# Performance work log

Hardware: AMD Instinct MI355X
Metric: run time of the kernel (lower is better)

The kernel has to match this reference:

```python
import math
import jax, jax.numpy as jnp
import numpy as np

B, T, D, M, S = 2, 4096, 1024, 256, 8
BEAM = 4
TAU = 1.0


def setup_inputs() -> dict:
    key = jax.random.key(0)
    ks = jax.random.split(key, 24)
    std = 0.02
    inp = {
        "mu": jax.random.normal(ks[0], (B, T, D), jnp.float32),
        "lam": jax.random.uniform(ks[1], (B, T, D), jnp.float32),
        "pi": jax.random.uniform(ks[2], (B, T, 7), jnp.float32),
        "pi_write": jax.random.uniform(ks[3], (B, T, 1), jnp.float32),
        "Wq": jax.random.normal(ks[4], (M, D), jnp.float32) * std,
        "bq": jnp.zeros((M,), jnp.float32),
        "Wk": jax.random.normal(ks[5], (M, D), jnp.float32) * std,
        "bk": jnp.zeros((M,), jnp.float32),
        "Wv": jax.random.normal(ks[6], (M, D), jnp.float32) * std,
        "bv": jnp.zeros((M,), jnp.float32),
        "Wo": jax.random.normal(ks[7], (D, M), jnp.float32) * std,
        "bo": jnp.zeros((D,), jnp.float32),
        "Ws1": jax.random.normal(ks[8], (256, 2 * D + 7), jnp.float32) * std,
        "bs1": jnp.zeros((256,), jnp.float32),
        "Ws2": jax.random.normal(ks[9], (1, 256), jnp.float32) * std,
        "bs2": jnp.zeros((1,), jnp.float32),
        "Wsr": jax.random.normal(ks[10], (M, M), jnp.float32) * std,
        "bsr": jnp.zeros((M,), jnp.float32),
        "scratch_init": jax.random.normal(ks[11], (1, S, M), jnp.float32) * 0.02,
        "gate": jnp.float32(-5.0),
    }
    return inp


def _build_tree(k, v, w):
    """Causal binary tree of weighted span summaries. Level 0 = leaves."""
    levels = [(k, v, w)]
    while k.shape[1] > 1:
        n = k.shape[1]
        if n % 2 == 1:
            pad = ((0, 0), (0, 1), (0, 0))
            k = jnp.pad(k, pad); v = jnp.pad(v, pad); w = jnp.pad(w, pad)
        k1, k2 = k[:, 0::2], k[:, 1::2]
        v1, v2 = v[:, 0::2], v[:, 1::2]
        w1, w2 = w[:, 0::2], w[:, 1::2]
        tw = w1 + w2 + 1e-8
        k = (w1 * k1 + w2 * k2) / tw
        v = (w1 * v1 + w2 * v2) / tw
        w = tw
        levels.append((k, v, w))
    return levels


def _retrieve_at_level(q, keys, values, beam):
    Bq, Tq, Mq = q.shape
    n = keys.shape[1]
    scores = jnp.einsum('btm,bnm->btn', q, keys) / math.sqrt(Mq)
    if n <= Tq:  # causal: query i may only see slot j <= i
        mask = jnp.arange(n)[None, :] > jnp.arange(Tq)[:, None]
        scores = jnp.where(mask[None], -jnp.inf, scores)
    kk = min(beam, n)
    if n > kk:
        vals, idx = jax.lax.top_k(scores, kk)           # (B,T,k)
        p = jax.nn.softmax(vals, axis=-1)               # == softmax of scattered sparse scores
        v_sel = jnp.take_along_axis(values[:, None], idx[..., None], axis=2)  # (B,T,k,M)
        return jnp.einsum('btk,btkm->btm', p, v_sel)
    attn = jax.nn.softmax(scores, axis=-1)
    return jnp.einsum('btn,bnm->btm', attn, values)


def reference(mu, lam, pi, pi_write, Wq, bq, Wk, bk, Wv, bv, Wo, bo,
              Ws1, bs1, Ws2, bs2, Wsr, bsr, scratch_init, gate):
    # ---- write: build causal tree from detached keys/values ----
    mu_d = jax.lax.stop_gradient(mu)
    w0 = jax.lax.stop_gradient(pi_write)                # (B,T,1)
    k = mu_d @ Wk.T + bk
    v = mu_d @ Wv.T + bv
    tree = _build_tree(k, v, w0)

    # ---- read ----
    q = mu @ Wq.T + bq                                  # (B,T,M)
    log_var = -jnp.log(jnp.clip(lam, 1e-6))
    si = jnp.concatenate([mu, log_var, pi], axis=-1)    # (B,T,2D+7)
    h = si @ Ws1.T + bs1
    h = h * jax.nn.sigmoid(h)                           # SiLU
    s = jax.nn.sigmoid((h @ Ws2.T + bs2)[..., 0])       # (B,T)

    scratch = jnp.broadcast_to(scratch_init, (mu.shape[0], S, M))
    sq = q @ Wsr.T + bsr
    sattn = jax.nn.softmax(jnp.einsum('btm,bsm->bts', sq, scratch) / math.sqrt(M), axis=-1)
    scratch_ctx = jnp.einsum('bts,bsm->btm', sattn, scratch)

    level_ctx = [_retrieve_at_level(q, lk, lv, BEAM) for (lk, lv, _) in tree]
    level_stack = jnp.stack(level_ctx, axis=2)          # (B,T,L,M)
    L = level_stack.shape[2]
    level_idx = jnp.arange(L, dtype=mu.dtype)
    s_scaled = s[..., None] * (L - 1)                   # (B,T,1)
    kappa = jnp.exp(-0.5 * ((level_idx - s_scaled) / TAU) ** 2)
    kappa = kappa / jnp.clip(kappa.sum(axis=-1, keepdims=True), 1e-8)
    tree_ctx = jnp.einsum('btl,btlm->btm', kappa, level_stack)

    blend = s[..., None]
    combined = (1.0 - blend) * tree_ctx + blend * scratch_ctx
    out = combined @ Wo.T + bo
    return jax.nn.sigmoid(gate) * out                   # (B,T,D)
```

## Files before the change

### kernel.cpp

```cpp
#include <hip/hip_runtime.h>
#include <math.h>

#define TT 4096
#define BB 2
#define MMDIM 256
#define RTOT 8192
#define NSLICE 39

typedef __attribute__((ext_vector_type(8))) short short8_t;
typedef __attribute__((ext_vector_type(4))) float f32x4;

__global__ __launch_bounds__(256) void gemm_f32(
    const float* __restrict__ A, const float* __restrict__ W,
    const float* __restrict__ bias, float* __restrict__ C, int K, int N)
{
    __shared__ float As[16][68];
    __shared__ float Ws[16][68];
    const int tid = threadIdx.x;
    const int tx = tid & 15, ty = tid >> 4;
    const int r0 = blockIdx.x * 64, c0 = blockIdx.y * 64;
    const int lr = tid >> 2;
    const int lk = (tid & 3) << 2;

    float acc[4][4] = {};

    for (int k0 = 0; k0 < K; k0 += 16) {
        float4 av = *(const float4*)&A[(size_t)(r0 + lr) * K + k0 + lk];
        float4 wv = *(const float4*)&W[(size_t)(c0 + lr) * K + k0 + lk];
        As[lk + 0][lr] = av.x; As[lk + 1][lr] = av.y;
        As[lk + 2][lr] = av.z; As[lk + 3][lr] = av.w;
        Ws[lk + 0][lr] = wv.x; Ws[lk + 1][lr] = wv.y;
        Ws[lk + 2][lr] = wv.z; Ws[lk + 3][lr] = wv.w;
        __syncthreads();
        #pragma unroll
        for (int kk = 0; kk < 16; ++kk) {
            float4 a = *(const float4*)&As[kk][ty * 4];
            float4 b = *(const float4*)&Ws[kk][tx * 4];
            acc[0][0] += a.x * b.x; acc[0][1] += a.x * b.y; acc[0][2] += a.x * b.z; acc[0][3] += a.x * b.w;
            acc[1][0] += a.y * b.x; acc[1][1] += a.y * b.y; acc[1][2] += a.y * b.z; acc[1][3] += a.y * b.w;
            acc[2][0] += a.z * b.x; acc[2][1] += a.z * b.y; acc[2][2] += a.z * b.z; acc[2][3] += a.z * b.w;
            acc[3][0] += a.w * b.x; acc[3][1] += a.w * b.y; acc[3][2] += a.w * b.z; acc[3][3] += a.w * b.w;
        }
        __syncthreads();
    }

    #pragma unroll
    for (int i = 0; i < 4; ++i) {
        int row = r0 + ty * 4 + i;
        float4 o;
        o.x = acc[i][0] + bias[c0 + tx * 4 + 0];
        o.y = acc[i][1] + bias[c0 + tx * 4 + 1];
        o.z = acc[i][2] + bias[c0 + tx * 4 + 2];
        o.w = acc[i][3] + bias[c0 + tx * 4 + 3];
        *(float4*)&C[(size_t)row * N + c0 + tx * 4] = o;
    }
}

__device__ __forceinline__ unsigned short f2bf(float x)
{
    unsigned u = __float_as_uint(x);
    u += 0x7fffu + ((u >> 16) & 1u);
    return (unsigned short)(u >> 16);
}

__global__ __launch_bounds__(256) void convert_split(
    const float* __restrict__ src, unsigned short* __restrict__ hi,
    unsigned short* __restrict__ lo, int n4)
{
    int i = blockIdx.x * 256 + threadIdx.x;
    if (i >= n4) return;
    float4 x = ((const float4*)src)[i];
    ushort4 h, l;
    h.x = f2bf(x.x); l.x = f2bf(x.x - __uint_as_float((unsigned)h.x << 16));
    h.y = f2bf(x.y); l.y = f2bf(x.y - __uint_as_float((unsigned)h.y << 16));
    h.z = f2bf(x.z); l.z = f2bf(x.z - __uint_as_float((unsigned)h.z << 16));
    h.w = f2bf(x.w); l.w = f2bf(x.w - __uint_as_float((unsigned)h.w << 16));
    ((ushort4*)hi)[i] = h;
    ((ushort4*)lo)[i] = l;
}

__global__ __launch_bounds__(256) void pad_ws1_split(
    const float* __restrict__ src, unsigned short* __restrict__ hi,
    unsigned short* __restrict__ lo)
{
    const int r = blockIdx.x;
    for (int c = threadIdx.x; c < 2112; c += 256) {
        float v = (c < 2055) ? src[(size_t)r * 2055 + c] : 0.f;
        unsigned short h = f2bf(v);
        hi[(size_t)r * 2112 + c] = h;
        lo[(size_t)r * 2112 + c] = f2bf(v - __uint_as_float((unsigned)h << 16));
    }
}

template<int ASRC, int WITH_GATE>
__global__ __launch_bounds__(256) void gemm_mfma(
    const float* __restrict__ A, const float* __restrict__ lam,
    const float* __restrict__ pi,
    const unsigned short* __restrict__ Wh, const unsigned short* __restrict__ Wl,
    const float* __restrict__ bias, const float* __restrict__ gate,
    float* __restrict__ C, int K, int N)
{
    __shared__ unsigned short Ah[64][72], Al[64][72];
    __shared__ unsigned short Bh[128][72], Bl[128][72];
    const int tid = threadIdx.x;
    const int lane = tid & 63;
    const int wv = tid >> 6;
    const int r0 = blockIdx.x * 64;
    const int c0 = blockIdx.y * 128;

    f32x4 acc0[8] = {}, acc1[8] = {}, acc2[8] = {};

    const int arow = wv * 16 + (lane & 15);
    const int koff = (lane >> 4) * 8;

    for (int kc = 0; kc < K; kc += 64) {
        #pragma unroll
        for (int i = 0; i < 2; ++i) {
            int g = tid + i * 256;
            int row = g >> 3, gq = g & 7;
            float x[8];
            if (ASRC == 0) {
                float4 v0 = *(const float4*)&A[(size_t)(r0 + row) * K + kc + gq * 8];
                float4 v1 = *(const float4*)&A[(size_t)(r0 + row) * K + kc + gq * 8 + 4];
                x[0] = v0.x; x[1] = v0.y; x[2] = v0.z; x[3] = v0.w;
                x[4] = v1.x; x[5] = v1.y; x[6] = v1.z; x[7] = v1.w;
            } else {
                #pragma unroll
                for (int e = 0; e < 8; ++e) {
                    int c = kc + gq * 8 + e;
                    float val;
                    if (c < 1024)      val = A[(size_t)(r0 + row) * 1024 + c];
                    else if (c < 2048) val = -logf(fmaxf(lam[(size_t)(r0 + row) * 1024 + (c - 1024)], 1e-6f));
                    else if (c < 2055) val = pi[(size_t)(r0 + row) * 7 + (c - 2048)];
                    else               val = 0.f;
                    x[e] = val;
                }
            }
            short8_t sh, sl;
            #pragma unroll
            for (int e = 0; e < 8; ++e) {
                unsigned short h = f2bf(x[e]);
                sh[e] = (short)h;
                sl[e] = (short)f2bf(x[e] - __uint_as_float((unsigned)h << 16));
            }
            *(short8_t*)&Ah[row][gq * 8] = sh;
            *(short8_t*)&Al[row][gq * 8] = sl;
        }
        #pragma unroll
        for (int i = 0; i < 4; ++i) {
            int g = tid + i * 256;
            int row = g >> 3, gq = g & 7;
            *(short8_t*)&Bh[row][gq * 8] = *(const short8_t*)&Wh[(size_t)(c0 + row) * K + kc + gq * 8];
            *(short8_t*)&Bl[row][gq * 8] = *(const short8_t*)&Wl[(size_t)(c0 + row) * K + kc + gq * 8];
        }
        __syncthreads();
        #pragma unroll
        for (int kt = 0; kt < 2; ++kt) {
            short8_t afh = *(const short8_t*)&Ah[arow][kt * 32 + koff];
            short8_t afl = *(const short8_t*)&Al[arow][kt * 32 + koff];
            #pragma unroll
            for (int ct = 0; ct < 8; ++ct) {
                short8_t bh = *(const short8_t*)&Bh[ct * 16 + (lane & 15)][kt * 32 + koff];
                short8_t bl = *(const short8_t*)&Bl[ct * 16 + (lane & 15)][kt * 32 + koff];
                acc0[ct] = __builtin_amdgcn_mfma_f32_16x16x32_bf16(afh, bh, acc0[ct], 0, 0, 0);
                acc1[ct] = __builtin_amdgcn_mfma_f32_16x16x32_bf16(afl, bh, acc1[ct], 0, 0, 0);
                acc2[ct] = __builtin_amdgcn_mfma_f32_16x16x32_bf16(afh, bl, acc2[ct], 0, 0, 0);
            }
        }
        __syncthreads();
    }

    float g = 1.f;
    if (WITH_GATE) g = 1.f / (1.f + expf(-gate[0]));
    #pragma unroll
    for (int ct = 0; ct < 8; ++ct) {
        int col = c0 + ct * 16 + (lane & 15);
        float b = bias[col];
        #pragma unroll
        for (int r = 0; r < 4; ++r) {
            int row = r0 + wv * 16 + (lane >> 4) * 4 + r;
            C[(size_t)row * N + col] = (acc0[ct][r] + acc1[ct][r] + acc2[ct][r] + b) * g;
        }
    }
}

__global__ __launch_bounds__(256) void s_kernel(
    const float* __restrict__ h, const float* __restrict__ Ws2,
    const float* __restrict__ bs2, float* __restrict__ sb,
    float* __restrict__ kap)
{
    const int tid = threadIdx.x;
    const int wave = tid >> 6, lane = tid & 63;
    const int t = blockIdx.x * 4 + wave;

    float4 hv = *(const float4*)&h[(size_t)t * MMDIM + lane * 4];
    float4 wv = *(const float4*)&Ws2[lane * 4];
    float p = 0.f;
    p += (hv.x / (1.f + expf(-hv.x))) * wv.x;
    p += (hv.y / (1.f + expf(-hv.y))) * wv.y;
    p += (hv.z / (1.f + expf(-hv.z))) * wv.z;
    p += (hv.w / (1.f + expf(-hv.w))) * wv.w;
    #pragma unroll
    for (int o = 32; o; o >>= 1) p += __shfl_xor(p, o);

    float z = p + bs2[0];
    float s = 1.f / (1.f + expf(-z));
    float c = s * 12.f;
    float Z = 0.f;
    #pragma unroll
    for (int l = 0; l < 13; ++l) {
        float d = (float)l - c;
        Z += expf(-0.5f * d * d);
    }
    Z = fmaxf(Z, 1e-8f);
    if (lane < 13) {
        float d = (float)lane - c;
        kap[(size_t)t * 16 + lane] = (1.f - s) * expf(-0.5f * d * d) / Z;
    }
    if (lane == 0) sb[t] = s;
}

__global__ __launch_bounds__(256) void scratch_kernel(
    const float* __restrict__ sq, const float* __restrict__ scr,
    const float* __restrict__ sb, float* __restrict__ ctx)
{
    const int tid = threadIdx.x;
    const int wave = tid >> 6, lane = tid & 63;
    const int t = blockIdx.x * 4 + wave;

    float4 qv = *(const float4*)&sq[(size_t)t * MMDIM + lane * 4];
    float4 fr[8];
    float sc[8];
    #pragma unroll
    for (int s = 0; s < 8; ++s) {
        fr[s] = *(const float4*)&scr[s * MMDIM + lane * 4];
        sc[s] = qv.x * fr[s].x + qv.y * fr[s].y + qv.z * fr[s].z + qv.w * fr[s].w;
    }
    #pragma unroll
    for (int s = 0; s < 8; ++s) {
        #pragma unroll
        for (int o = 32; o; o >>= 1) sc[s] += __shfl_xor(sc[s], o);
        sc[s] *= 0.0625f;
    }
    float mx = sc[0];
    #pragma unroll
    for (int s = 1; s < 8; ++s) mx = fmaxf(mx, sc[s]);
    float sum = 0.f;
    #pragma unroll
    for (int s = 0; s < 8; ++s) { sc[s] = expf(sc[s] - mx); sum += sc[s]; }
    float inv = 1.f / sum;
    float blend = sb[t];
    float4 o = {0, 0, 0, 0};
    #pragma unroll
    for (int s = 0; s < 8; ++s) {
        float pp = sc[s] * inv;
        o.x += pp * fr[s].x; o.y += pp * fr[s].y;
        o.z += pp * fr[s].z; o.w += pp * fr[s].w;
    }
    o.x *= blend; o.y *= blend; o.z *= blend; o.w *= blend;
    *(float4*)&ctx[(size_t)t * MMDIM + lane * 4] = o;
}

__global__ __launch_bounds__(256) void wtree_kernel(
    const float* __restrict__ pw, float* __restrict__ wtree)
{
    __shared__ float wa[4096];
    __shared__ float wb2[2048];
    const int b = blockIdx.x;
    const int tid = threadIdx.x;
    for (int t = tid; t < 4096; t += 256) wa[t] = pw[b * 4096 + t];
    __syncthreads();
    int n = 4096, lvl = 1;
    float* cur = wa; float* nxt = wb2;
    while (n > 1) {
        int nout = n >> 1;
        int off = TT - (8192 >> lvl);
        for (int j = tid; j < nout; j += 256) {
            float t = cur[2 * j] + cur[2 * j + 1] + 1e-8f;
            nxt[j] = t;
            wtree[b * 4095 + off + j] = t;
        }
        __syncthreads();
        float* tmp = cur; cur = nxt; nxt = tmp;
        n = nout; ++lvl;
    }
}

__global__ __launch_bounds__(256) void tree_level(
    const float* __restrict__ kin, const float* __restrict__ vin,
    const float* __restrict__ win, float* __restrict__ kout,
    float* __restrict__ vout, int in_bs, int win_bs, int out_bs)
{
    const int j = blockIdx.x;
    const int b = blockIdx.y;
    const int tid = threadIdx.x;
    const float* wp = win + (size_t)b * win_bs;
    float w1 = wp[2 * j], w2 = wp[2 * j + 1];
    float tw = w1 + w2 + 1e-8f;
    size_t i1 = ((size_t)b * in_bs + 2 * j) * MMDIM + tid;
    size_t io = ((size_t)b * out_bs + j) * MMDIM + tid;
    kout[io] = (w1 * kin[i1] + w2 * kin[i1 + MMDIM]) / tw;
    vout[io] = (w1 * vin[i1] + w2 * vin[i1 + MMDIM]) / tw;
}

__global__ __launch_bounds__(256) void tree_mid(
    float* __restrict__ kt_, float* __restrict__ vt_,
    const float* __restrict__ wtree)
{
    __shared__ float kb[128][68];
    __shared__ float vb[128][68];
    const int tid = threadIdx.x;
    const int g  = blockIdx.x >> 2;
    const int mc = blockIdx.x & 3;
    const int b  = blockIdx.y;
    const int wb = b * 4095;

    for (int idx = tid; idx < 64 * 64; idx += 256) {
        int j = idx >> 6, m = idx & 63;
        size_t gi = (size_t)(wb + g * 64 + j) * MMDIM + mc * 64 + m;
        kb[j][m] = kt_[gi];
        vb[j][m] = vt_[gi];
    }
    __syncthreads();

    int pb = 0;
    for (int l = 2; l <= 6; ++l) {
        int nloc = 64 >> (l - 1);
        int cb = 128 - (128 >> (l - 1));
        int offm1 = TT - (8192 >> (l - 1));
        int offl  = TT - (8192 >> l);
        int gbase = g * nloc;
        for (int idx = tid; idx < nloc * 64; idx += 256) {
            int j = idx >> 6, m = idx & 63;
            float w1 = wtree[wb + offm1 + (gbase + j) * 2];
            float w2 = wtree[wb + offm1 + (gbase + j) * 2 + 1];
            float tw = wtree[wb + offl + gbase + j];
            float kvv = (w1 * kb[pb + 2 * j][m] + w2 * kb[pb + 2 * j + 1][m]) / tw;
            float vvv = (w1 * vb[pb + 2 * j][m] + w2 * vb[pb + 2 * j + 1][m]) / tw;
            kb[cb + j][m] = kvv;
            vb[cb + j][m] = vvv;
            size_t go = (size_t)(wb + offl + gbase + j) * MMDIM + mc * 64 + m;
            kt_[go] = kvv;
            vt_[go] = vvv;
        }
        __syncthreads();
        pb = cb;
    }
}

__global__ __launch_bounds__(256) void tree_deep(
    float* __restrict__ kt_, float* __restrict__ vt_,
    const float* __restrict__ wtree)
{
    __shared__ float kb[128][68];
    __shared__ float vb[128][68];
    const int tid = threadIdx.x;
    const int mc = blockIdx.x;
    const int b = blockIdx.y;
    const int wb = b * 4095;

    for (int idx = tid; idx < 64 * 64; idx += 256) {
        int j = idx >> 6, m = idx & 63;
        size_t gi = (size_t)(wb + 3968 + j) * MMDIM + mc * 64 + m;
        kb[j][m] = kt_[gi];
        vb[j][m] = vt_[gi];
    }
    __syncthreads();

    int pb = 0;
    for (int l = 7; l <= 12; ++l) {
        int nout = 4096 >> l;
        int cb = 128 - (128 >> (l - 6));
        int offm1 = TT - (8192 >> (l - 1));
        int offl  = TT - (8192 >> l);
        for (int idx = tid; idx < nout * 64; idx += 256) {
            int j = idx >> 6, m = idx & 63;
            float w1 = wtree[wb + offm1 + 2 * j];
            float w2 = wtree[wb + offm1 + 2 * j + 1];
            float tw = wtree[wb + offl + j];
            float kvv = (w1 * kb[pb + 2 * j][m] + w2 * kb[pb + 2 * j + 1][m]) / tw;
            float vvv = (w1 * vb[pb + 2 * j][m] + w2 * vb[pb + 2 * j + 1][m]) / tw;
            kb[cb + j][m] = kvv;
            vb[cb + j][m] = vvv;
            size_t go = (size_t)(wb + offl + j) * MMDIM + mc * 64 + m;
            kt_[go] = kvv;
            vt_[go] = vvv;
        }
        __syncthreads();
        pb = cb;
    }
}

__device__ __forceinline__ unsigned long long pack_key(float v, int col)
{
    unsigned u = __float_as_uint(v);
    u ^= ((unsigned)((int)u >> 31)) | 0x80000000u;
    return ((unsigned long long)u << 32) | (unsigned)(~col);
}

__device__ __forceinline__ void unpack_key(unsigned long long k, float& v, int& col)
{
    unsigned u = (unsigned)(k >> 32);
    u ^= (u & 0x80000000u) ? 0x80000000u : 0xFFFFFFFFu;
    v = __uint_as_float(u);
    col = (int)(~(unsigned)k);
}

__device__ __forceinline__ unsigned long long shfl_xor_u64(unsigned long long v, int off)
{
    int lo = __shfl_xor((int)(unsigned)v, off);
    int hi = __shfl_xor((int)(v >> 32), off);
    return ((unsigned long long)(unsigned)hi << 32) | (unsigned)lo;
}

__device__ __forceinline__ void ins4u(unsigned long long k, unsigned long long t[4])
{
    if (k <= t[3]) return;
    t[3] = k;
    if (t[3] > t[2]) { unsigned long long x = t[2]; t[2] = t[3]; t[3] = x; }
    if (t[2] > t[1]) { unsigned long long x = t[1]; t[1] = t[2]; t[2] = x; }
    if (t[1] > t[0]) { unsigned long long x = t[0]; t[0] = t[1]; t[1] = x; }
}

__device__ __forceinline__ void ins5u(unsigned long long k, unsigned long long t[5])
{
    if (k <= t[4]) return;
    t[4] = k;
    if (t[4] > t[3]) { unsigned long long x = t[3]; t[3] = t[4]; t[4] = x; }
    if (t[3] > t[2]) { unsigned long long x = t[2]; t[2] = t[3]; t[3] = x; }
    if (t[2] > t[1]) { unsigned long long x = t[1]; t[1] = t[2]; t[2] = x; }
    if (t[1] > t[0]) { unsigned long long x = t[0]; t[0] = t[1]; t[1] = x; }
}

__device__ __forceinline__ bool beats(float v, int id, float v2, int id2)
{
    return (v > v2) || (v == v2 && id < id2);
}

__device__ __forceinline__ void ins5(float v, int id, float tv[5], int ti[5])
{
    if (!beats(v, id, tv[4], ti[4])) return;
    tv[4] = v; ti[4] = id;
    #pragma unroll
    for (int s = 4; s > 0; --s) {
        if (beats(tv[s], ti[s], tv[s - 1], ti[s - 1])) {
            float fv = tv[s]; tv[s] = tv[s - 1]; tv[s - 1] = fv;
            int iv = ti[s]; ti[s] = ti[s - 1]; ti[s - 1] = iv;
        }
    }
}

__device__ __forceinline__ void slice_map(int sid, int& level, int& c0)
{
    if (sid < 16)      { level = 0; c0 = sid << 8; }
    else if (sid < 24) { level = 1; c0 = (sid - 16) << 8; }
    else if (sid < 28) { level = 2; c0 = (sid - 24) << 8; }
    else if (sid < 30) { level = 3; c0 = (sid - 28) << 8; }
    else               { level = sid - 26; c0 = 0; }
}

__global__ __launch_bounds__(512) void topk_mfma(
    const unsigned short* __restrict__ qkh, const unsigned short* __restrict__ qkl,
    const unsigned short* __restrict__ kth, const unsigned short* __restrict__ ktl,
    float2* __restrict__ topw)
{
    __shared__ unsigned short kbh[32][264];
    __shared__ unsigned short kbl[32][264];

    const int tid = threadIdx.x;
    const int lane = tid & 63;
    const int wv = tid >> 6;
    const int r0 = blockIdx.x * 128;
    const int sid = blockIdx.y;
    const int b = r0 >> 12;
    const int t0 = r0 & 4095;

    int level, c0b;
    slice_map(sid, level, c0b);
    const int n = TT >> level;
    const int nv = min(min(n, t0 + 128), c0b + 256);

    if (c0b >= nv) {
        if (tid < 128) {
            float2 e = make_float2(-INFINITY, __int_as_float(0x7fffffff));
            #pragma unroll
            for (int s = 0; s < 5; ++s)
                topw[(size_t)(sid * 5 + s) * RTOT + r0 + tid] = e;
        }
        return;
    }

    const unsigned short* Kh;
    const unsigned short* Kl;
    if (level == 0) {
        Kh = qkh + (size_t)RTOT * MMDIM + (size_t)b * TT * MMDIM;
        Kl = qkl + (size_t)RTOT * MMDIM + (size_t)b * TT * MMDIM;
    } else {
        size_t off = (size_t)b * 4095 + (TT - (8192 >> level));
        Kh = kth + off * MMDIM;
        Kl = ktl + off * MMDIM;
    }

    const int arow = r0 + wv * 16 + (lane & 15);
    const int koff = (lane >> 4) * 8;
    short8_t ah[8], al[8];
    #pragma unroll
    for (int kt = 0; kt < 8; ++kt) {
        ah[kt] = *(const short8_t*)(qkh + (size_t)arow * MMDIM + kt * 32 + koff);
        al[kt] = *(const short8_t*)(qkl + (size_t)arow * MMDIM + kt * 32 + koff);
    }

    unsigned long long tk[4][4] = {};
    const int trow0 = t0 + wv * 16 + (lane >> 4) * 4;

    const int scol = tid >> 4;
    const int kseg = (tid & 15) * 16;

    for (int c0 = c0b; c0 < nv; c0 += 32) {
        {
            int cc = min(c0 + scol, n - 1);
            const unsigned short* gh = Kh + (size_t)cc * MMDIM + kseg;
            const unsigned short* gl = Kl + (size_t)cc * MMDIM + kseg;
            *(short8_t*)&kbh[scol][kseg]     = *(const short8_t*)gh;
            *(short8_t*)&kbh[scol][kseg + 8] = *(const short8_t*)(gh + 8);
            *(short8_t*)&kbl[scol][kseg]     = *(const short8_t*)gl;
            *(short8_t*)&kbl[scol][kseg + 8] = *(const short8_t*)(gl + 8);
        }
        __syncthreads();

        #pragma unroll
        for (int ct = 0; ct < 2; ++ct) {
            f32x4 a0 = {0.f, 0.f, 0.f, 0.f};
            f32x4 a1 = {0.f, 0.f, 0.f, 0.f};
            f32x4 a2 = {0.f, 0.f, 0.f, 0.f};
            const int bc = ct * 16 + (lane & 15);
            #pragma unroll
            for (int kt = 0; kt < 8; ++kt) {
                short8_t bh = *(const short8_t*)&kbh[bc][kt * 32 + koff];
                short8_t bl = *(const short8_t*)&kbl[bc][kt * 32 + koff];
                a0 = __builtin_amdgcn_mfma_f32_16x16x32_bf16(ah[kt], bh, a0, 0, 0, 0);
                a1 = __builtin_amdgcn_mfma_f32_16x16x32_bf16(al[kt], bh, a1, 0, 0, 0);
                a2 = __builtin_amdgcn_mfma_f32_16x16x32_bf16(ah[kt], bl, a2, 0, 0, 0);
            }
            const int col = c0 + bc;
            #pragma unroll
            for (int r = 0; r < 4; ++r) {
                float sc = (a0[r] + a1[r] + a2[r]) * 0.0625f;
                unsigned long long key =
                    (col <= trow0 + r && col < n) ? pack_key(sc, col) : 0ull;
                if (__any(key > tk[r][3])) ins4u(key, tk[r]);
            }
        }
        __syncthreads();
    }

    #pragma unroll
    for (int r = 0; r < 4; ++r) {
        unsigned long long k5[5];
        #pragma unroll
        for (int s = 0; s < 4; ++s) k5[s] = tk[r][s];
        k5[4] = 0ull;
        #pragma unroll
        for (int pass = 0; pass < 4; ++pass) {
            int off = 1 << pass;
            unsigned long long o[5];
            #pragma unroll
            for (int s = 0; s < 5; ++s) o[s] = shfl_xor_u64(k5[s], off);
            #pragma unroll
            for (int s = 0; s < 5; ++s) ins5u(o[s], k5);
        }
        if ((lane & 15) == 0) {
            int row = r0 + wv * 16 + (lane >> 4) * 4 + r;
            #pragma unroll
            for (int s = 0; s < 5; ++s) {
                float2 e;
                if (k5[s] == 0ull) {
                    e = make_float2(-INFINITY, __int_as_float(0x7fffffff));
                } else {
                    float v; int c;
                    unpack_key(k5[s], v, c);
                    e = make_float2(v, __int_as_float(c));
                }
                topw[(size_t)(sid * 5 + s) * RTOT + row] = e;
            }
        }
    }
}

__global__ __launch_bounds__(256) void merge_gather(
    const float2* __restrict__ topw, const float* __restrict__ q,
    const float* __restrict__ kl0, const float* __restrict__ ktf,
    const float* __restrict__ vl0, const float* __restrict__ vtree,
    const float* __restrict__ kap, float* __restrict__ ctx)
{
    const int tid = threadIdx.x;
    const int lane = tid & 63;
    const int wv = __builtin_amdgcn_readfirstlane(tid >> 6);
    const int row = blockIdx.x * 4 + wv;
    const int b = row >> 12;

    float cr[4] = {0, 0, 0, 0};
    const float4 q4 = *(const float4*)&q[(size_t)row * MMDIM + lane * 4];

    for (int l = 0; l <= 12; ++l) {
        int s0, cnt;
        if (l == 0)      { s0 = 0;  cnt = 16; }
        else if (l == 1) { s0 = 16; cnt = 8; }
        else if (l == 2) { s0 = 24; cnt = 4; }
        else if (l == 3) { s0 = 28; cnt = 2; }
        else             { s0 = 26 + l; cnt = 1; }

        float tv[5]; int ti[5];
        #pragma unroll
        for (int s = 0; s < 5; ++s) { tv[s] = -INFINITY; ti[s] = 0x7fffffff; }
        for (int sl = 0; sl < cnt; ++sl) {
            #pragma unroll
            for (int s = 0; s < 5; ++s) {
                float2 e = topw[(size_t)((s0 + sl) * 5 + s) * RTOT + row];
                if (e.x > -INFINITY) ins5(e.x, __float_as_int(e.y), tv, ti);
            }
        }

        const float* Kf = (l == 0)
            ? kl0 + (size_t)b * TT * MMDIM
            : ktf + ((size_t)b * 4095 + (TT - (8192 >> l))) * MMDIM;

        bool ambig = (l <= 9) && (tv[3] - tv[4] < 1e-4f);
        if (ambig) {
            float rv[5]; int ri[5];
            #pragma unroll
            for (int s = 0; s < 5; ++s) { rv[s] = -INFINITY; ri[s] = 0x7fffffff; }
            for (int sl = 0; sl < cnt; ++sl) {
                #pragma unroll
                for (int s = 0; s < 5; ++s) {
                    float2 e = topw[(size_t)((s0 + sl) * 5 + s) * RTOT + row];
                    if (e.x > -INFINITY) {
                        int idx = __float_as_int(e.y);
                        float4 k4 = *(const float4*)&Kf[(size_t)idx * MMDIM + lane * 4];
                        float p = q4.x * k4.x + q4.y * k4.y + q4.z * k4.z + q4.w * k4.w;
                        #pragma unroll
                        for (int o = 32; o; o >>= 1) p += __shfl_xor(p, o);
                        ins5(p * 0.0625f, idx, rv, ri);
                    }
                }
            }
            #pragma unroll
            for (int s = 0; s < 5; ++s) { tv[s] = rv[s]; ti[s] = ri[s]; }
        }

        float m0 = tv[0];
        float e0 = expf(tv[0] - m0);
        float e1 = expf(tv[1] - m0);
        float e2 = expf(tv[2] - m0);
        float e3 = expf(tv[3] - m0);
        float sum = e0 + e1 + e2 + e3;
        float kp = kap[(size_t)row * 16 + l];
        float scl = kp / sum;
        float ps[4] = {e0 * scl, e1 * scl, e2 * scl, e3 * scl};

        const float* Vb = (l == 0)
            ? vl0 + (size_t)b * TT * MMDIM
            : vtree + ((size_t)b * 4095 + (TT - (8192 >> l))) * MMDIM;

        #pragma unroll
        for (int s = 0; s < 4; ++s) {
            if (ps[s] > 0.f) {
                float4 vv = *(const float4*)&Vb[(size_t)ti[s] * MMDIM + lane * 4];
                cr[0] += ps[s] * vv.x; cr[1] += ps[s] * vv.y;
                cr[2] += ps[s] * vv.z; cr[3] += ps[s] * vv.w;
            }
        }
    }

    float* cp = ctx + (size_t)row * MMDIM + lane * 4;
    float4 c = *(float4*)cp;
    c.x += cr[0]; c.y += cr[1]; c.z += cr[2]; c.w += cr[3];
    *(float4*)cp = c;
}

extern "C" void kernel_launch(void* const* d_in, const int* in_sizes, int n_in,
                              void* d_out, int out_size, void* d_ws, size_t ws_size,
                              hipStream_t stream)
{
    const float* mu  = (const float*)d_in[0];
    const float* lam = (const float*)d_in[1];
    const float* pi  = (const float*)d_in[2];
    const float* pw  = (const float*)d_in[3];
    const float* Wq  = (const float*)d_in[4];
    const float* bq  = (const float*)d_in[5];
    const float* Wk  = (const float*)d_in[6];
    const float* bk  = (const float*)d_in[7];
    const float* Wv  = (const float*)d_in[8];
    const float* bv  = (const float*)d_in[9];
    const float* Wo  = (const float*)d_in[10];
    const float* bo  = (const float*)d_in[11];
    const float* Ws1 = (const float*)d_in[12];
    const float* bs1 = (const float*)d_in[13];
    const float* Ws2 = (const float*)d_in[14];
    const float* bs2 = (const float*)d_in[15];
    const float* Wsr = (const float*)d_in[16];
    const float* bsr = (const float*)d_in[17];
    const float* scr = (const float*)d_in[18];
    const float* gate = (const float*)d_in[19];
    float* out = (float*)d_out;

    float* w = (float*)d_ws;
    const size_t RM = (size_t)RTOT * MMDIM;
    float* q_   = w;  w += RM;
    float* k_   = w;  w += RM;
    float* v_   = w;  w += RM;
    float* h_   = w;  w += RM;
    float* sq_  = w;  w += RM;
    float* ctx_ = w;  w += RM;
    float* sb_  = w;  w += RTOT;
    float* kap_ = w;  w += (size_t)RTOT * 16;
    float* kt_  = w;  w += (size_t)BB * 4095 * MMDIM;
    float* vt_  = w;  w += (size_t)BB * 4095 * MMDIM;
    float* wtree_ = w; w += (size_t)BB * 4095;
    unsigned short* qkh_ = (unsigned short*)w;  w += RM;
    unsigned short* qkl_ = (unsigned short*)w;  w += RM;
    unsigned short* kth_ = (unsigned short*)w;  w += (size_t)BB * 4095 * MMDIM / 2;
    unsigned short* ktl_ = (unsigned short*)w;  w += (size_t)BB * 4095 * MMDIM / 2;
    float2* topw = (float2*)w;  w += (size_t)NSLICE * 5 * RTOT * 2;
    unsigned short* w1h_ = (unsigned short*)w;  w += (size_t)256 * 2112 / 2;
    unsigned short* w1l_ = (unsigned short*)w;  w += (size_t)256 * 2112 / 2;
    unsigned short* wvh_ = (unsigned short*)w;  w += (size_t)256 * 1024 / 2;
    unsigned short* wvl_ = (unsigned short*)w;  w += (size_t)256 * 1024 / 2;
    unsigned short* wsrh_ = (unsigned short*)w; w += (size_t)256 * 256 / 2;
    unsigned short* wsrl_ = (unsigned short*)w; w += (size_t)256 * 256 / 2;
    unsigned short* woh_ = (unsigned short*)w;  w += (size_t)1024 * 256 / 2;
    unsigned short* wol_ = (unsigned short*)w;  w += (size_t)1024 * 256 / 2;

    pad_ws1_split<<<256, 256, 0, stream>>>(Ws1, w1h_, w1l_);
    convert_split<<<256, 256, 0, stream>>>(Wv, wvh_, wvl_, 65536);
    convert_split<<<64, 256, 0, stream>>>(Wsr, wsrh_, wsrl_, 16384);
    convert_split<<<256, 256, 0, stream>>>(Wo, woh_, wol_, 65536);

    gemm_f32<<<dim3(128, 4), 256, 0, stream>>>(mu, Wq, bq, q_, 1024, 256);
    gemm_f32<<<dim3(128, 4), 256, 0, stream>>>(mu, Wk, bk, k_, 1024, 256);
    gemm_mfma<0, 0><<<dim3(128, 2), 256, 0, stream>>>(mu, nullptr, nullptr, wvh_, wvl_,
                                                      bv, nullptr, v_, 1024, 256);
    gemm_mfma<1, 0><<<dim3(128, 2), 256, 0, stream>>>(mu, lam, pi, w1h_, w1l_,
                                                      bs1, nullptr, h_, 2112, 256);
    s_kernel<<<2048, 256, 0, stream>>>(h_, Ws2, bs2, sb_, kap_);
    gemm_mfma<0, 0><<<dim3(128, 2), 256, 0, stream>>>(q_, nullptr, nullptr, wsrh_, wsrl_,
                                                      bsr, nullptr, sq_, 256, 256);
    scratch_kernel<<<2048, 256, 0, stream>>>(sq_, scr, sb_, ctx_);

    wtree_kernel<<<BB, 256, 0, stream>>>(pw, wtree_);
    tree_level<<<dim3(2048, BB), 256, 0, stream>>>(k_, v_, pw, kt_, vt_,
                                                   TT, TT, 4095);
    tree_mid<<<dim3(128, BB), 256, 0, stream>>>(kt_, vt_, wtree_);
    tree_deep<<<dim3(4, BB), 256, 0, stream>>>(kt_, vt_, wtree_);

    convert_split<<<(int)((2 * RM / 4 + 255) / 256), 256, 0, stream>>>(
        q_, qkh_, qkl_, (int)(2 * RM / 4));
    convert_split<<<(int)(((size_t)BB * 4095 * MMDIM / 4 + 255) / 256), 256, 0, stream>>>(
        kt_, kth_, ktl_, (int)((size_t)BB * 4095 * MMDIM / 4));

    topk_mfma<<<dim3(64, NSLICE), 512, 0, stream>>>(qkh_, qkl_, kth_, ktl_, topw);
    merge_gather<<<2048, 256, 0, stream>>>(topw, q_, k_, kt_, v_, vt_, kap_, ctx_);
    gemm_mfma<0, 1><<<dim3(128, 8), 256, 0, stream>>>(ctx_, nullptr, nullptr, woh_, wol_,
                                                      bo, gate, out, 256, 1024);
}
```

Measured before the change: 899.9 us.

## Fuse Q/K projections with bf16 split conversion and double-buffer top-k tiles

Replaces the two separate fp32 GEMM launches for Q and K with one kernel that uses 64x128 tiles, register-prefetched double-buffered shared memory, and writes the hi/lo bf16 split of q and k directly. This removes one convert_split pass over q/k and one kernel launch. The top-k MFMA kernel also gains double-buffered LDS for key tiles, prefetching the next tile into registers while computing the current one, so it needs only one barrier per iteration. The cost is doubled LDS use in topk_mfma, which may reduce occupancy.

```diff
diff --git a/kernel.cpp b/kernel.cpp
--- a/kernel.cpp
+++ b/kernel.cpp
@@ -10,57 +10,104 @@
 typedef __attribute__((ext_vector_type(8))) short short8_t;
 typedef __attribute__((ext_vector_type(4))) float f32x4;
 
-__global__ __launch_bounds__(256) void gemm_f32(
-    const float* __restrict__ A, const float* __restrict__ W,
-    const float* __restrict__ bias, float* __restrict__ C, int K, int N)
-{
-    __shared__ float As[16][68];
-    __shared__ float Ws[16][68];
-    const int tid = threadIdx.x;
-    const int tx = tid & 15, ty = tid >> 4;
-    const int r0 = blockIdx.x * 64, c0 = blockIdx.y * 64;
-    const int lr = tid >> 2;
-    const int lk = (tid & 3) << 2;
-
-    float acc[4][4] = {};
-
-    for (int k0 = 0; k0 < K; k0 += 16) {
-        float4 av = *(const float4*)&A[(size_t)(r0 + lr) * K + k0 + lk];
-        float4 wv = *(const float4*)&W[(size_t)(c0 + lr) * K + k0 + lk];
-        As[lk + 0][lr] = av.x; As[lk + 1][lr] = av.y;
-        As[lk + 2][lr] = av.z; As[lk + 3][lr] = av.w;
-        Ws[lk + 0][lr] = wv.x; Ws[lk + 1][lr] = wv.y;
-        Ws[lk + 2][lr] = wv.z; Ws[lk + 3][lr] = wv.w;
-        __syncthreads();
-        #pragma unroll
-        for (int kk = 0; kk < 16; ++kk) {
-            float4 a = *(const float4*)&As[kk][ty * 4];
-            float4 b = *(const float4*)&Ws[kk][tx * 4];
-            acc[0][0] += a.x * b.x; acc[0][1] += a.x * b.y; acc[0][2] += a.x * b.z; acc[0][3] += a.x * b.w;
-            acc[1][0] += a.y * b.x; acc[1][1] += a.y * b.y; acc[1][2] += a.y * b.z; acc[1][3] += a.y * b.w;
-            acc[2][0] += a.z * b.x; acc[2][1] += a.z * b.y; acc[2][2] += a.z * b.z; acc[2][3] += a.z * b.w;
-            acc[3][0] += a.w * b.x; acc[3][1] += a.w * b.y; acc[3][2] += a.w * b.z; acc[3][3] += a.w * b.w;
-        }
-        __syncthreads();
-    }
-
-    #pragma unroll
-    for (int i = 0; i < 4; ++i) {
-        int row = r0 + ty * 4 + i;
-        float4 o;
-        o.x = acc[i][0] + bias[c0 + tx * 4 + 0];
-        o.y = acc[i][1] + bias[c0 + tx * 4 + 1];
-        o.z = acc[i][2] + bias[c0 + tx * 4 + 2];
-        o.w = acc[i][3] + bias[c0 + tx * 4 + 3];
-        *(float4*)&C[(size_t)row * N + c0 + tx * 4] = o;
-    }
-}
-
 __device__ __forceinline__ unsigned short f2bf(float x)
 {
     unsigned u = __float_as_uint(x);
     u += 0x7fffu + ((u >> 16) & 1u);
     return (unsigned short)(u >> 16);
+}
+
+__global__ __launch_bounds__(256) void gemm_qk(
+    const float* __restrict__ mu, const float* __restrict__ Wq,
+    const float* __restrict__ bq, const float* __restrict__ Wk,
+    const float* __restrict__ bk, float* __restrict__ q_, float* __restrict__ k_,
+    unsigned short* __restrict__ qkh, unsigned short* __restrict__ qkl)
+{
+    __shared__ float As[2][8][68];
+    __shared__ float Ws[2][8][132];
+    const int tid = threadIdx.x;
+    const int tx = tid & 15;
+    const int ty = tid >> 4;
+    const int r0 = blockIdx.x * 64;
+    const int c0 = blockIdx.y * 128;
+    const bool isq = (c0 < 256);
+
+    const float* W = isq ? (Wq + (size_t)c0 * 1024)
+                         : (Wk + (size_t)(c0 - 256) * 1024);
+    const float* bias = isq ? (bq + c0) : (bk + (c0 - 256));
+
+    const bool isA = (tid < 128);
+    const int sArow = tid >> 1, sAk = (tid & 1) * 4;
+    const int sWrow = tid >> 1, sWk = (tid & 1) * 4;
+
+    float acc[4][8] = {};
+    float4 rA, rW;
+
+    if (isA) rA = *(const float4*)&mu[(size_t)(r0 + sArow) * 1024 + sAk];
+    rW = *(const float4*)&W[(size_t)sWrow * 1024 + sWk];
+    if (isA) {
+        As[0][sAk + 0][sArow] = rA.x; As[0][sAk + 1][sArow] = rA.y;
+        As[0][sAk + 2][sArow] = rA.z; As[0][sAk + 3][sArow] = rA.w;
+    }
+    Ws[0][sWk + 0][sWrow] = rW.x; Ws[0][sWk + 1][sWrow] = rW.y;
+    Ws[0][sWk + 2][sWrow] = rW.z; Ws[0][sWk + 3][sWrow] = rW.w;
+    __syncthreads();
+
+    int buf = 0;
+    for (int k0 = 0; k0 < 1024; k0 += 8) {
+        const bool has = (k0 + 8 < 1024);
+        if (has) {
+            if (isA) rA = *(const float4*)&mu[(size_t)(r0 + sArow) * 1024 + k0 + 8 + sAk];
+            rW = *(const float4*)&W[(size_t)sWrow * 1024 + k0 + 8 + sWk];
+        }
+        #pragma unroll
+        for (int kk = 0; kk < 8; ++kk) {
+            float4 a  = *(const float4*)&As[buf][kk][ty * 4];
+            float4 b0 = *(const float4*)&Ws[buf][kk][tx * 8];
+            float4 b1 = *(const float4*)&Ws[buf][kk][tx * 8 + 4];
+            float av[4] = {a.x, a.y, a.z, a.w};
+            float bv[8] = {b0.x, b0.y, b0.z, b0.w, b1.x, b1.y, b1.z, b1.w};
+            #pragma unroll
+            for (int i = 0; i < 4; ++i)
+                #pragma unroll
+                for (int j = 0; j < 8; ++j)
+                    acc[i][j] += av[i] * bv[j];
+        }
+        if (has) {
+            int nb = buf ^ 1;
+            if (isA) {
+                As[nb][sAk + 0][sArow] = rA.x; As[nb][sAk + 1][sArow] = rA.y;
+                As[nb][sAk + 2][sArow] = rA.z; As[nb][sAk + 3][sArow] = rA.w;
+            }
+            Ws[nb][sWk + 0][sWrow] = rW.x; Ws[nb][sWk + 1][sWrow] = rW.y;
+            Ws[nb][sWk + 2][sWrow] = rW.z; Ws[nb][sWk + 3][sWrow] = rW.w;
+        }
+        __syncthreads();
+        buf ^= 1;
+    }
+
+    const int lcol = (c0 & 255) + tx * 8;
+    #pragma unroll
+    for (int i = 0; i < 4; ++i) {
+        int row = r0 + ty * 4 + i;
+        float o[8];
+        #pragma unroll
+        for (int j = 0; j < 8; ++j) o[j] = acc[i][j] + bias[tx * 8 + j];
+        float* dst = isq ? &q_[(size_t)row * MMDIM + lcol]
+                         : &k_[(size_t)row * MMDIM + lcol];
+        *(float4*)dst       = make_float4(o[0], o[1], o[2], o[3]);
+        *(float4*)(dst + 4) = make_float4(o[4], o[5], o[6], o[7]);
+        size_t srow = isq ? (size_t)row : (size_t)(RTOT + row);
+        short8_t sh, sl;
+        #pragma unroll
+        for (int j = 0; j < 8; ++j) {
+            unsigned short h = f2bf(o[j]);
+            sh[j] = (short)h;
+            sl[j] = (short)f2bf(o[j] - __uint_as_float((unsigned)h << 16));
+        }
+        *(short8_t*)&qkh[srow * MMDIM + lcol] = sh;
+        *(short8_t*)&qkl[srow * MMDIM + lcol] = sl;
+    }
 }
 
 __global__ __launch_bounds__(256) void convert_split(
@@ -464,8 +511,8 @@
     const unsigned short* __restrict__ kth, const unsigned short* __restrict__ ktl,
     float2* __restrict__ topw)
 {
-    __shared__ unsigned short kbh[32][264];
-    __shared__ unsigned short kbl[32][264];
+    __shared__ unsigned short kbh[2][32][264];
+    __shared__ unsigned short kbl[2][32][264];
 
     const int tid = threadIdx.x;
     const int lane = tid & 63;
@@ -516,17 +563,30 @@
     const int scol = tid >> 4;
     const int kseg = (tid & 15) * 16;
 
+    short8_t nh0, nh1, nl0, nl1;
+    {
+        int cc = min(c0b + scol, n - 1);
+        const unsigned short* gh = Kh + (size_t)cc * MMDIM + kseg;
+        const unsigned short* gl = Kl + (size_t)cc * MMDIM + kseg;
+        nh0 = *(const short8_t*)gh; nh1 = *(const short8_t*)(gh + 8);
+        nl0 = *(const short8_t*)gl; nl1 = *(const short8_t*)(gl + 8);
+    }
+    *(short8_t*)&kbh[0][scol][kseg]     = nh0;
+    *(short8_t*)&kbh[0][scol][kseg + 8] = nh1;
+    *(short8_t*)&kbl[0][scol][kseg]     = nl0;
+    *(short8_t*)&kbl[0][scol][kseg + 8] = nl1;
+    __syncthreads();
+
+    int buf = 0;
     for (int c0 = c0b; c0 < nv; c0 += 32) {
-        {
-            int cc = min(c0 + scol, n - 1);
+        const bool has = (c0 + 32 < nv);
+        if (has) {
+            int cc = min(c0 + 32 + scol, n - 1);
             const unsigned short* gh = Kh + (size_t)cc * MMDIM + kseg;
             const unsigned short* gl = Kl + (size_t)cc * MMDIM + kseg;
-            *(short8_t*)&kbh[scol][kseg]     = *(const short8_t*)gh;
-            *(short8_t*)&kbh[scol][kseg + 8] = *(const short8_t*)(gh + 8);
-            *(short8_t*)&kbl[scol][kseg]     = *(const short8_t*)gl;
-            *(short8_t*)&kbl[scol][kseg + 8] = *(const short8_t*)(gl + 8);
-        }
-        __syncthreads();
+            nh0 = *(const short8_t*)gh; nh1 = *(const short8_t*)(gh + 8);
+            nl0 = *(const short8_t*)gl; nl1 = *(const short8_t*)(gl + 8);
+        }
 
         #pragma unroll
         for (int ct = 0; ct < 2; ++ct) {
@@ -536,8 +596,8 @@
             const int bc = ct * 16 + (lane & 15);
             #pragma unroll
             for (int kt = 0; kt < 8; ++kt) {
-                short8_t bh = *(const short8_t*)&kbh[bc][kt * 32 + koff];
-                short8_t bl = *(const short8_t*)&kbl[bc][kt * 32 + koff];
+                short8_t bh = *(const short8_t*)&kbh[buf][bc][kt * 32 + koff];
+                short8_t bl = *(const short8_t*)&kbl[buf][bc][kt * 32 + koff];
                 a0 = __builtin_amdgcn_mfma_f32_16x16x32_bf16(ah[kt], bh, a0, 0, 0, 0);
                 a1 = __builtin_amdgcn_mfma_f32_16x16x32_bf16(al[kt], bh, a1, 0, 0, 0);
                 a2 = __builtin_amdgcn_mfma_f32_16x16x32_bf16(ah[kt], bl, a2, 0, 0, 0);
@@ -551,7 +611,16 @@
                 if (__any(key > tk[r][3])) ins4u(key, tk[r]);
             }
         }
+
+        if (has) {
+            int nb = buf ^ 1;
+            *(short8_t*)&kbh[nb][scol][kseg]     = nh0;
+            *(short8_t*)&kbh[nb][scol][kseg + 8] = nh1;
+            *(short8_t*)&kbl[nb][scol][kseg]     = nl0;
+            *(short8_t*)&kbl[nb][scol][kseg + 8] = nl1;
+        }
         __syncthreads();
+        buf ^= 1;
     }
 
     #pragma unroll
@@ -736,8 +805,8 @@
     convert_split<<<64, 256, 0, stream>>>(Wsr, wsrh_, wsrl_, 16384);
     convert_split<<<256, 256, 0, stream>>>(Wo, woh_, wol_, 65536);
 
-    gemm_f32<<<dim3(128, 4), 256, 0, stream>>>(mu, Wq, bq, q_, 1024, 256);
-    gemm_f32<<<dim3(128, 4), 256, 0, stream>>>(mu, Wk, bk, k_, 1024, 256);
+    gemm_qk<<<dim3(128, 4), 256, 0, stream>>>(mu, Wq, bq, Wk, bk,
+                                              q_, k_, qkh_, qkl_);
     gemm_mfma<0, 0><<<dim3(128, 2), 256, 0, stream>>>(mu, nullptr, nullptr, wvh_, wvl_,
                                                       bv, nullptr, v_, 1024, 256);
     gemm_mfma<1, 0><<<dim3(128, 2), 256, 0, stream>>>(mu, lam, pi, w1h_, w1l_,
@@ -753,8 +822,6 @@
     tree_mid<<<dim3(128, BB), 256, 0, stream>>>(kt_, vt_, wtree_);
     tree_deep<<<dim3(4, BB), 256, 0, stream>>>(kt_, vt_, wtree_);
 
-    convert_split<<<(int)((2 * RM / 4 + 255) / 256), 256, 0, stream>>>(
-        q_, qkh_, qkl_, (int)(2 * RM / 4));
     convert_split<<<(int)(((size_t)BB * 4095 * MMDIM / 4 + 255) / 256), 256, 0, stream>>>(
         kt_, kth_, ktl_, (int)((size_t)BB * 4095 * MMDIM / 4));
 
```

Result: faster. 838.4 us (-6.8%).
